# Kernel optimization log

Measured on AMD Instinct MI355X. Metric: run time of the kernel, lower is better.

## Reference

```python
import jax, jax.numpy as jnp
import numpy as np

D_MODEL = 1024
N_HEADS = 16
HEAD_DIM = D_MODEL // N_HEADS  # 64
SEQ = 2048
BATCH = 2


def setup_inputs() -> dict:
    key = jax.random.key(0)
    ks = jax.random.split(key, 12)
    s = 1.0 / np.sqrt(D_MODEL)
    return {
        "query": jax.random.normal(ks[0], (SEQ, BATCH, D_MODEL), jnp.float32),
        "key": jax.random.normal(ks[1], (SEQ, BATCH, D_MODEL), jnp.float32),
        "value": jax.random.normal(ks[2], (SEQ, BATCH, D_MODEL), jnp.float32),
        "Wq": jax.random.normal(ks[3], (D_MODEL, D_MODEL), jnp.float32) * s,
        "bq": jax.random.normal(ks[4], (D_MODEL,), jnp.float32) * s,
        "Wk": jax.random.normal(ks[5], (D_MODEL, D_MODEL), jnp.float32) * s,
        "bk": jax.random.normal(ks[6], (D_MODEL,), jnp.float32) * s,
        "Wv": jax.random.normal(ks[7], (D_MODEL, D_MODEL), jnp.float32) * s,
        "bv": jax.random.normal(ks[8], (D_MODEL,), jnp.float32) * s,
        "Wo": jax.random.normal(ks[9], (D_MODEL, D_MODEL), jnp.float32) * s,
        "bo": jax.random.normal(ks[10], (D_MODEL,), jnp.float32) * s,
    }


def _rope_tables(seq_len):
    # theta_i = 1 / 10000^(2i/head_dim), i in [0, head_dim//2)
    theta = 1.0 / (10000.0 ** (2.0 * jnp.arange(HEAD_DIM // 2, dtype=jnp.float32) / HEAD_DIM))
    pos = jnp.arange(seq_len, dtype=jnp.float32)[:, None, None, None] * theta  # [S,1,1,hd/2]
    return jnp.sin(pos), jnp.cos(pos)


def _apply_rope(t, sin, cos):
    # t: [S, B, H, hd]; NOTE faithful to source: t2 = q1*sin - q2*cos (minus)
    h = HEAD_DIM // 2
    q1, q2 = t[..., :h], t[..., h:]
    return jnp.concatenate([q1 * cos - q2 * sin, q1 * sin - q2 * cos], axis=-1)


def reference(query, key, value, Wq, bq, Wk, bk, Wv, bv, Wo, bo):
    S, B, _ = query.shape
    q = (query @ Wq.T + bq).reshape(S, B, N_HEADS, HEAD_DIM)
    k = (key @ Wk.T + bk).reshape(S, B, N_HEADS, HEAD_DIM)
    v = (value @ Wv.T + bv).reshape(S, B, N_HEADS, HEAD_DIM)
    sin, cos = _rope_tables(S)
    q = _apply_rope(q, sin, cos)
    k = _apply_rope(k, sin, cos)
    # [S,B,H,d] -> [B,H,S,d]
    q = q.transpose(1, 2, 0, 3)
    k = k.transpose(1, 2, 0, 3)
    v = v.transpose(1, 2, 0, 3)
    scale = 1.0 / jnp.sqrt(jnp.float32(HEAD_DIM))
    scores = jnp.einsum("bhqd,bhkd->bhqk", q, k) * scale
    attn = jax.nn.softmax(scores, axis=-1)
    out = jnp.einsum("bhqk,bhkd->bhqd", attn, v)  # [B,H,S,d]
    out = out.transpose(2, 0, 1, 3).reshape(S, B, D_MODEL)
    return out @ Wo.T + bo
```

## Files before the change

kernel.cpp:

```cpp
#include <hip/hip_runtime.h>

#define DMODEL 1024
#define NHEADS 16
#define HDIM   64
#define SEQ    2048
#define BATCH  2
#define MROWS  (SEQ*BATCH)

typedef unsigned int u32;
typedef unsigned short u16;
typedef __attribute__((ext_vector_type(8))) short bfrag;
typedef __attribute__((ext_vector_type(4))) float f32x4;
typedef __attribute__((ext_vector_type(16))) float f32x16;
typedef union { u32 u[4]; bfrag f; } fragu;

__device__ __forceinline__ u32 f2bf(float x) {
    unsigned u = __float_as_uint(x);
    return (u + 0x7fffu + ((u >> 16) & 1u)) >> 16;
}
__device__ __forceinline__ float bf2f(u32 h) {
    return __uint_as_float(h << 16);
}
__device__ __forceinline__ u32 packbf(float x) {
    const u32 h = f2bf(x);
    const u32 l = f2bf(x - bf2f(h));
    return h | (l << 16);
}

__device__ __forceinline__ void gld16(const void* g, void* l) {
    __builtin_amdgcn_global_load_lds(
        (const __attribute__((address_space(1))) unsigned int*)g,
        (__attribute__((address_space(3))) unsigned int*)l, 16, 0, 0);
}

__device__ __forceinline__ void unpack8(uint4 x, uint4 y, bfrag& hi, bfrag& lo) {
    fragu h, l;
    const u32 pk[8] = {x.x, x.y, x.z, x.w, y.x, y.y, y.z, y.w};
    #pragma unroll
    for (int j = 0; j < 4; ++j) {
        h.u[j] = (pk[2 * j] & 0xffffu) | (pk[2 * j + 1] << 16);
        l.u[j] = (pk[2 * j] >> 16) | (pk[2 * j + 1] & 0xffff0000u);
    }
    hi = h.f; lo = l.f;
}

__global__ __launch_bounds__(256) void prep_kernel(
    const float* __restrict__ Wq, const float* __restrict__ Wk,
    const float* __restrict__ Wv,
    float* __restrict__ query, float* __restrict__ key, float* __restrict__ value,
    u32* __restrict__ wqp, u32* __restrict__ wkp, u32* __restrict__ wvp,
    float2* __restrict__ tab)
{
    const int y = blockIdx.y;
    if (y == 3) {
        if (blockIdx.x >= 256) return;
        const int e = blockIdx.x * 256 + threadIdx.x;
        const int s = e >> 5, i = e & 31;
        const double th = exp(-(double)i * (9.210340371976184 / 32.0));
        double sn, cs;
        sincos((double)s * th, &sn, &cs);
        tab[e] = make_float2((float)sn, (float)cs);
        return;
    }
    const float* src; u32* dst;
    if (y < 3) {
        if (blockIdx.x >= 512) return;
        src = (y == 0) ? Wq : (y == 1) ? Wk : Wv;
        dst = (y == 0) ? wqp : (y == 1) ? wkp : wvp;
    } else {
        float* io = (y == 4) ? query : (y == 5) ? key : value;
        src = io;
        dst = (u32*)io;
    }
    const int i = blockIdx.x * 256 + threadIdx.x;
    float xs[8];
    *(float4*)&xs[0] = ((const float4*)src)[i * 2];
    *(float4*)&xs[4] = ((const float4*)src)[i * 2 + 1];
    u32 p[8];
    #pragma unroll
    for (int j = 0; j < 8; ++j) p[j] = packbf(xs[j]);
    *(uint4*)&dst[i * 8]     = *(const uint4*)&p[0];
    *(uint4*)&dst[i * 8 + 4] = *(const uint4*)&p[4];
}

__global__ __launch_bounds__(256) void pack_kernel(
    const float* __restrict__ src, u32* __restrict__ dst)
{
    const int i = blockIdx.x * 256 + threadIdx.x;
    float xs[8];
    *(float4*)&xs[0] = ((const float4*)src)[i * 2];
    *(float4*)&xs[4] = ((const float4*)src)[i * 2 + 1];
    u32 p[8];
    #pragma unroll
    for (int j = 0; j < 8; ++j) p[j] = packbf(xs[j]);
    *(uint4*)&dst[i * 8]     = *(const uint4*)&p[0];
    *(uint4*)&dst[i * 8 + 4] = *(const uint4*)&p[4];
}

__device__ __forceinline__ void gemm_body(
    int id, int mode,
    const u32* __restrict__ Ap, const u32* __restrict__ Wp,
    const float* __restrict__ bias, const float2* __restrict__ tab,
    float rope_scale,
    u16* __restrict__ Oh, u16* __restrict__ Ol, float* __restrict__ Of,
    u32* smem)
{
    u32* sA = smem;
    u32* sB = smem + 8192;

    const int tid   = threadIdx.x;
    const int w     = tid >> 6;
    const int lane  = tid & 63;
    const int lrow  = lane & 15;
    const int lquad = lane >> 4;

    const int xcd  = id & 7;
    const int jj   = id >> 3;
    const int nblk = jj & 15;
    const int mblk = (xcd << 2) | (jj >> 4);
    const int n0   = nblk * 64;
    const int m0   = mblk * 128;

    const int srow8 = lane >> 3;
    const int sch   = (lane & 7) ^ srow8;

    int aoff[2][2];
    int boff[4][2];
    #pragma unroll
    for (int mi = 0; mi < 2; ++mi) {
        const int ra = w * 32 + mi * 16 + lrow;
        #pragma unroll
        for (int hf = 0; hf < 2; ++hf)
            aoff[mi][hf] = ra * 32 + (((lquad * 2 + hf) ^ (ra & 7)) << 2);
    }
    #pragma unroll
    for (int ni = 0; ni < 4; ++ni) {
        const int rb = ni * 16 + lrow;
        #pragma unroll
        for (int hf = 0; hf < 2; ++hf)
            boff[ni][hf] = rb * 32 + (((lquad * 2 + hf) ^ (rb & 7)) << 2);
    }

    f32x4 acc[2][4] = {};

    auto stage = [&](int t) {
        const int h  = t & 1;
        const int kc = t * 32;
        #pragma unroll
        for (int i = 0; i < 4; ++i) {
            const int slab = w * 4 + i;
            const int row  = slab * 8 + srow8;
            gld16(Ap + (size_t)(m0 + row) * 1024 + kc + sch * 4,
                  sA + h * 4096 + slab * 256);
        }
        #pragma unroll
        for (int i = 0; i < 2; ++i) {
            const int slab = w * 2 + i;
            const int row  = slab * 8 + srow8;
            gld16(Wp + (size_t)(n0 + row) * 1024 + kc + sch * 4,
                  sB + h * 2048 + slab * 256);
        }
    };

    stage(0);
    for (int t = 0; t < 32; ++t) {
        __syncthreads();
        if (t < 31) stage(t + 1);
        const int h = t & 1;
        const u32* sAh_ = sA + h * 4096;
        const u32* sBh_ = sB + h * 2048;

        bfrag ah[2], al[2], bh[4], bl[4];
        #pragma unroll
        for (int mi = 0; mi < 2; ++mi)
            unpack8(*(const uint4*)(sAh_ + aoff[mi][0]),
                    *(const uint4*)(sAh_ + aoff[mi][1]), ah[mi], al[mi]);
        #pragma unroll
        for (int ni = 0; ni < 4; ++ni)
            unpack8(*(const uint4*)(sBh_ + boff[ni][0]),
                    *(const uint4*)(sBh_ + boff[ni][1]), bh[ni], bl[ni]);

        #pragma unroll
        for (int mi = 0; mi < 2; ++mi)
            #pragma unroll
            for (int ni = 0; ni < 4; ++ni) {
                acc[mi][ni] = __builtin_amdgcn_mfma_f32_16x16x32_bf16(ah[mi], bh[ni], acc[mi][ni], 0, 0, 0);
                acc[mi][ni] = __builtin_amdgcn_mfma_f32_16x16x32_bf16(ah[mi], bl[ni], acc[mi][ni], 0, 0, 0);
                acc[mi][ni] = __builtin_amdgcn_mfma_f32_16x16x32_bf16(al[mi], bh[ni], acc[mi][ni], 0, 0, 0);
            }
    }

    float bn[4];
    #pragma unroll
    for (int ni = 0; ni < 4; ++ni) bn[ni] = bias[n0 + ni * 16 + lrow];

    if (mode == 0) {
        const int hblk = nblk;
        #pragma unroll
        for (int mi = 0; mi < 2; ++mi)
            #pragma unroll
            for (int r = 0; r < 4; ++r) {
                const int mrow = w * 32 + mi * 16 + lquad * 4 + r;
                const int m  = m0 + mrow;
                const int bb = m & 1;
                const int sg = m >> 1;
                const size_t ob = (((size_t)(bb * NHEADS + hblk) * SEQ) + sg) * HDIM;
                #pragma unroll
                for (int ni = 0; ni < 2; ++ni) {
                    const int i = ni * 16 + lrow;
                    const float2 sc = tab[(size_t)sg * 32 + i];
                    const float x1 = acc[mi][ni][r]     + bn[ni];
                    const float x2 = acc[mi][ni + 2][r] + bn[ni + 2];
                    const float o1 = (x1 * sc.y - x2 * sc.x) * rope_scale;
                    const float o2 = (x1 * sc.x - x2 * sc.y) * rope_scale;
                    const u32 h1 = f2bf(o1);
                    const u32 h2 = f2bf(o2);
                    Oh[ob + i]      = (u16)h1;  Ol[ob + i]      = (u16)f2bf(o1 - bf2f(h1));
                    Oh[ob + i + 32] = (u16)h2;  Ol[ob + i + 32] = (u16)f2bf(o2 - bf2f(h2));
                }
            }
    } else if (mode == 1) {
        __syncthreads();
        u32* vb = smem;
        #pragma unroll
        for (int mi = 0; mi < 2; ++mi)
            #pragma unroll
            for (int r = 0; r < 4; ++r) {
                const int mrow = w * 32 + mi * 16 + lquad * 4 + r;
                const int bb = mrow & 1;
                const int sl = mrow >> 1;
                #pragma unroll
                for (int ni = 0; ni < 4; ++ni) {
                    const int d = ni * 16 + lrow;
                    vb[bb * 4160 + d * 65 + sl] = f2bf(acc[mi][ni][r] + bn[ni]);
                }
            }
        __syncthreads();
        const int hblk = nblk;
        #pragma unroll
        for (int rep = 0; rep < 4; ++rep) {
            const int c  = rep * 256 + tid;
            const int bb = c >> 9;
            const int d  = (c >> 3) & 63;
            const int s8 = c & 7;
            __align__(8) u16 hb[8];
            #pragma unroll
            for (int j = 0; j < 8; ++j)
                hb[j] = (u16)vb[bb * 4160 + d * 65 + s8 * 8 + j];
            const size_t orow = ((size_t)(bb * NHEADS + hblk) * HDIM + d) * SEQ + (m0 >> 1);
            const int blk16 = (s8 >> 1) * 16;
            const int off   = (s8 & 1) * 4;
            *(uint2*)&Oh[orow + blk16 + off]     = *(const uint2*)&hb[0];
            *(uint2*)&Oh[orow + blk16 + 8 + off] = *(const uint2*)&hb[4];
        }
    } else {
        #pragma unroll
        for (int mi = 0; mi < 2; ++mi)
            #pragma unroll
            for (int r = 0; r < 4; ++r) {
                const int m = m0 + w * 32 + mi * 16 + lquad * 4 + r;
                #pragma unroll
                for (int ni = 0; ni < 4; ++ni)
                    Of[(size_t)m * 1024 + n0 + ni * 16 + lrow] = acc[mi][ni][r] + bn[ni];
            }
    }
}

__global__ __launch_bounds__(256) void qkv_gemm_kernel(
    const u32* __restrict__ query, const u32* __restrict__ key,
    const u32* __restrict__ value,
    const u32* __restrict__ Wqp, const u32* __restrict__ Wkp,
    const u32* __restrict__ Wvp,
    const float* __restrict__ bq, const float* __restrict__ bk,
    const float* __restrict__ bv, const float2* __restrict__ tab,
    u16* __restrict__ Qh, u16* __restrict__ Ql,
    u16* __restrict__ Kh, u16* __restrict__ Kl,
    u16* __restrict__ VTh)
{
    __shared__ uint4 smem4[3072];
    const int z  = blockIdx.z;
    const int id = blockIdx.x + 16 * blockIdx.y;
    const u32* A    = (z == 0) ? query : (z == 1) ? key : value;
    const u32* Wp   = (z == 0) ? Wqp : (z == 1) ? Wkp : Wvp;
    const float* bb = (z == 0) ? bq : (z == 1) ? bk : bv;
    u16* Oh = (z == 0) ? Qh : (z == 1) ? Kh : VTh;
    u16* Ol = (z == 0) ? Ql : (z == 1) ? Kl : nullptr;
    const int mode = (z == 2) ? 1 : 0;
    const float scale = (z == 0) ? 0.125f : 1.0f;
    gemm_body(id, mode, A, Wp, bb, tab, scale, Oh, Ol, nullptr, (u32*)smem4);
}

__global__ __launch_bounds__(256) void out_gemm_kernel(
    const u32* __restrict__ Ap, const u32* __restrict__ Wp,
    const float* __restrict__ bias, float* __restrict__ Of)
{
    __shared__ uint4 smem4[3072];
    const int id = blockIdx.x + 16 * blockIdx.y;
    gemm_body(id, 2, Ap, Wp, bias, nullptr, 1.0f, nullptr, nullptr, Of, (u32*)smem4);
}

__global__ __launch_bounds__(256) void attn_mfma_kernel(
    const u16* __restrict__ Qh, const u16* __restrict__ Ql,
    const u16* __restrict__ Kh, const u16* __restrict__ Kl,
    const u16* __restrict__ Vh,
    u32* __restrict__ AOp)
{
    __shared__ u16 sKh[8192], sKl[8192];
    __shared__ u16 sVh[8192];

    const int tid  = threadIdx.x;
    const int w    = tid >> 6;
    const int lane = tid & 63;
    const int l31  = lane & 31;
    const int g    = lane >> 5;

    const int id = blockIdx.x + 16 * blockIdx.y;
    const int jj = id >> 3;
    const int bh = ((id & 7) << 2) | (jj >> 4);
    const int qt = jj & 15;

    const size_t qg = ((size_t)bh * SEQ + qt * 128 + w * 32 + l31) * HDIM + g * 8;
    bfrag qfh[4], qfl[4];
    #pragma unroll
    for (int ks = 0; ks < 4; ++ks) {
        qfh[ks] = *(const bfrag*)&Qh[qg + ks * 16];
        qfl[ks] = *(const bfrag*)&Ql[qg + ks * 16];
    }

    const int srow   = lane >> 3;
    const int schunk = (lane & 7) ^ srow;
    const u16* gsrc = nullptr; u16* lbase = nullptr; size_t istep = 0, ktstep = 0;
    if (w == 0) {
        gsrc = Kh + ((size_t)bh * SEQ + srow) * HDIM + schunk * 8;
        istep = 8 * 64; ktstep = 64 * 64; lbase = sKh;
    } else if (w == 1) {
        gsrc = Kl + ((size_t)bh * SEQ + srow) * HDIM + schunk * 8;
        istep = 8 * 64; ktstep = 64 * 64; lbase = sKl;
    } else if (w == 2) {
        gsrc = Vh + ((size_t)bh * HDIM + srow) * SEQ + schunk * 8;
        istep = 8 * SEQ; ktstep = 64; lbase = sVh;
    }

    int koff[2][4];
    #pragma unroll
    for (int a = 0; a < 2; ++a) {
        const int row = a * 32 + l31;
        #pragma unroll
        for (int c = 0; c < 4; ++c)
            koff[a][c] = row * 64 + (((c * 2 + g) ^ (row & 7)) << 3);
    }

    f32x16 accO[2] = {};
    float l_loc = 0.0f;

    auto stage = [&](int kt) {
        if (w < 3) {
            const u16* gp = gsrc + (size_t)kt * ktstep;
            u16* dst = lbase + (kt & 1) * 4096;
            #pragma unroll
            for (int i = 0; i < 8; ++i)
                gld16(gp + (size_t)i * istep, dst + i * 512);
        }
    };

    stage(0);
    for (int kt = 0; kt < SEQ / 64; ++kt) {
        __syncthreads();
        if (kt < SEQ / 64 - 1) stage(kt + 1);
        const int po = (kt & 1) * 4096;

        f32x16 accS[2] = {};
        #pragma unroll
        for (int kg = 0; kg < 2; ++kg)
            #pragma unroll
            for (int ks = 0; ks < 4; ++ks) {
                const bfrag kh = *(const bfrag*)&sKh[po + koff[kg][ks]];
                const bfrag kl = *(const bfrag*)&sKl[po + koff[kg][ks]];
                accS[kg] = __builtin_amdgcn_mfma_f32_32x32x16_bf16(kh, qfh[ks], accS[kg], 0, 0, 0);
                accS[kg] = __builtin_amdgcn_mfma_f32_32x32x16_bf16(kh, qfl[ks], accS[kg], 0, 0, 0);
                accS[kg] = __builtin_amdgcn_mfma_f32_32x32x16_bf16(kl, qfh[ks], accS[kg], 0, 0, 0);
            }

        float pv[2][16];
        #pragma unroll
        for (int kg = 0; kg < 2; ++kg)
            #pragma unroll
            for (int r = 0; r < 16; ++r) {
                const float p = __expf(accS[kg][r]);
                pv[kg][r] = p;
                l_loc += p;
            }

        #pragma unroll
        for (int kp = 0; kp < 4; ++kp) {
            const int kg = kp >> 1;
            const int t8 = (kp & 1) * 8;
            fragu ph;
            #pragma unroll
            for (int j2 = 0; j2 < 4; ++j2)
                ph.u[j2] = f2bf(pv[kg][t8 + 2 * j2]) |
                           (f2bf(pv[kg][t8 + 2 * j2 + 1]) << 16);
            #pragma unroll
            for (int dt = 0; dt < 2; ++dt) {
                const bfrag vh = *(const bfrag*)&sVh[po + koff[dt][kp]];
                accO[dt] = __builtin_amdgcn_mfma_f32_32x32x16_bf16(vh, ph.f, accO[dt], 0, 0, 0);
            }
        }
    }

    const float inv = 1.0f / (l_loc + __shfl_xor(l_loc, 32));

    const int b = bh >> 4;
    const int h = bh & 15;
    const int sg = qt * 128 + w * 32 + l31;
    const size_t obase = ((size_t)sg * BATCH + b) * DMODEL + h * 64;
    #pragma unroll
    for (int dt = 0; dt < 2; ++dt)
        #pragma unroll
        for (int rq = 0; rq < 4; ++rq) {
            const int d0 = 8 * rq + 4 * g + 32 * dt;
            uint4 pw;
            pw.x = packbf(accO[dt][rq * 4 + 0] * inv);
            pw.y = packbf(accO[dt][rq * 4 + 1] * inv);
            pw.z = packbf(accO[dt][rq * 4 + 2] * inv);
            pw.w = packbf(accO[dt][rq * 4 + 3] * inv);
            *(uint4*)&AOp[obase + d0] = pw;
        }
}

extern "C" void kernel_launch(void* const* d_in, const int* in_sizes, int n_in,
                              void* d_out, int out_size, void* d_ws, size_t ws_size,
                              hipStream_t stream)
{
    float* query = (float*)d_in[0];
    float* key   = (float*)d_in[1];
    float* value = (float*)d_in[2];
    const float* Wq    = (const float*)d_in[3];
    const float* bq    = (const float*)d_in[4];
    const float* Wk    = (const float*)d_in[5];
    const float* bk    = (const float*)d_in[6];
    const float* Wv    = (const float*)d_in[7];
    const float* bv    = (const float*)d_in[8];
    const float* Wo    = (const float*)d_in[9];
    const float* bo    = (const float*)d_in[10];
    float* out = (float*)d_out;

    char* wsb = (char*)d_ws;
    const size_t MB = 1024 * 1024;
    u32* Wqp = (u32*)(wsb + 0 * MB);
    u32* Wkp = (u32*)(wsb + 4 * MB);
    u32* Wvp = (u32*)(wsb + 8 * MB);
    float2* tab = (float2*)(wsb + 12 * MB);
    u16* Qh  = (u16*)(wsb + 16 * MB); u16* Ql  = (u16*)(wsb + 24 * MB);
    u16* Kh  = (u16*)(wsb + 32 * MB); u16* Kl  = (u16*)(wsb + 40 * MB);
    u16* VTh = (u16*)(wsb + 48 * MB);
    u32* AOp = (u32*)(wsb + 0 * MB);
    u32* Wop = (u32*)(wsb + 16 * MB);

    prep_kernel<<<dim3(2048, 7), 256, 0, stream>>>(
        Wq, Wk, Wv, query, key, value, Wqp, Wkp, Wvp, tab);
    qkv_gemm_kernel<<<dim3(16, 32, 3), 256, 0, stream>>>(
        (const u32*)query, (const u32*)key, (const u32*)value,
        Wqp, Wkp, Wvp, bq, bk, bv, tab,
        Qh, Ql, Kh, Kl, VTh);
    attn_mfma_kernel<<<dim3(16, 32), 256, 0, stream>>>(
        Qh, Ql, Kh, Kl, VTh, AOp);
    pack_kernel<<<512, 256, 0, stream>>>(Wo, Wop);
    out_gemm_kernel<<<dim3(16, 32), 256, 0, stream>>>(AOp, Wop, bo, out);
}
```

Measured before the change: 335.1 us.

## Split attention KV range across blocks, pre-split bf16 hi/lo layout, narrower out GEMM tiles

Operands are now stored as separate bf16 hi and lo halves in 32-element chunks, so the GEMM loads MFMA fragments directly without per-iteration unpacking. Attention splits the key range in two via blockIdx.z and accumulates unnormalized outputs and row sums with float atomics into zeroed buffers. A new combine kernel normalizes and packs the result. The output GEMM uses 32-column tiles to launch twice as many blocks. In exchange this adds extra kernels, atomic traffic, and drops the double-buffered K/V staging in attention.

```diff
diff --git a/kernel.cpp b/kernel.cpp
--- a/kernel.cpp
+++ b/kernel.cpp
@@ -21,11 +21,6 @@
 __device__ __forceinline__ float bf2f(u32 h) {
     return __uint_as_float(h << 16);
 }
-__device__ __forceinline__ u32 packbf(float x) {
-    const u32 h = f2bf(x);
-    const u32 l = f2bf(x - bf2f(h));
-    return h | (l << 16);
-}
 
 __device__ __forceinline__ void gld16(const void* g, void* l) {
     __builtin_amdgcn_global_load_lds(
@@ -33,22 +28,12 @@
         (__attribute__((address_space(3))) unsigned int*)l, 16, 0, 0);
 }
 
-__device__ __forceinline__ void unpack8(uint4 x, uint4 y, bfrag& hi, bfrag& lo) {
-    fragu h, l;
-    const u32 pk[8] = {x.x, x.y, x.z, x.w, y.x, y.y, y.z, y.w};
-    #pragma unroll
-    for (int j = 0; j < 4; ++j) {
-        h.u[j] = (pk[2 * j] & 0xffffu) | (pk[2 * j + 1] << 16);
-        l.u[j] = (pk[2 * j] >> 16) | (pk[2 * j + 1] & 0xffff0000u);
-    }
-    hi = h.f; lo = l.f;
-}
 
 __global__ __launch_bounds__(256) void prep_kernel(
     const float* __restrict__ Wq, const float* __restrict__ Wk,
     const float* __restrict__ Wv,
     float* __restrict__ query, float* __restrict__ key, float* __restrict__ value,
-    u32* __restrict__ wqp, u32* __restrict__ wkp, u32* __restrict__ wvp,
+    u16* __restrict__ wqb, u16* __restrict__ wkb, u16* __restrict__ wvb,
     float2* __restrict__ tab)
 {
     const int y = blockIdx.y;
@@ -62,51 +47,92 @@
         tab[e] = make_float2((float)sn, (float)cs);
         return;
     }
-    const float* src; u32* dst;
     if (y < 3) {
-        if (blockIdx.x >= 512) return;
-        src = (y == 0) ? Wq : (y == 1) ? Wk : Wv;
-        dst = (y == 0) ? wqp : (y == 1) ? wkp : wvp;
-    } else {
-        float* io = (y == 4) ? query : (y == 5) ? key : value;
-        src = io;
-        dst = (u32*)io;
-    }
+        const float* src = (y == 0) ? Wq : (y == 1) ? Wk : Wv;
+        u16* dst = (y == 0) ? wqb : (y == 1) ? wkb : wvb;
+        const int i = blockIdx.x * 256 + threadIdx.x;
+        const int e0  = i * 8;
+        const int row = e0 >> 10, k = e0 & 1023, t = k >> 5, j0 = k & 31;
+        float xs[8];
+        *(float4*)&xs[0] = ((const float4*)src)[i * 2];
+        *(float4*)&xs[4] = ((const float4*)src)[i * 2 + 1];
+        __align__(16) u16 hb[8];
+        __align__(16) u16 lb[8];
+        #pragma unroll
+        for (int j = 0; j < 8; ++j) {
+            const u32 h = f2bf(xs[j]);
+            hb[j] = (u16)h;
+            lb[j] = (u16)f2bf(xs[j] - bf2f(h));
+        }
+        u16* o = dst + (size_t)row * 2048 + t * 64 + j0;
+        *(uint4*)o        = *(const uint4*)hb;
+        *(uint4*)(o + 32) = *(const uint4*)lb;
+        return;
+    }
+    float* io = (y == 4) ? query : (y == 5) ? key : value;
+    const int gi = blockIdx.x * 256 + threadIdx.x;
+    uint4* io4 = (uint4*)io + (size_t)gi * 8;
+    uint4 raw[8];
+    #pragma unroll
+    for (int j = 0; j < 8; ++j) raw[j] = io4[j];
+    __align__(16) u16 hb[32];
+    __align__(16) u16 lb[32];
+    #pragma unroll
+    for (int j = 0; j < 32; ++j) {
+        const float x = __uint_as_float(((const u32*)raw)[j]);
+        const u32 h = f2bf(x);
+        hb[j] = (u16)h;
+        lb[j] = (u16)f2bf(x - bf2f(h));
+    }
+    #pragma unroll
+    for (int j = 0; j < 4; ++j) io4[j]     = ((const uint4*)hb)[j];
+    #pragma unroll
+    for (int j = 0; j < 4; ++j) io4[4 + j] = ((const uint4*)lb)[j];
+}
+
+__global__ __launch_bounds__(256) void pack_kernel(
+    const float* __restrict__ src, u16* __restrict__ dst)
+{
     const int i = blockIdx.x * 256 + threadIdx.x;
+    const int e0  = i * 8;
+    const int row = e0 >> 10, k = e0 & 1023, t = k >> 5, j0 = k & 31;
     float xs[8];
     *(float4*)&xs[0] = ((const float4*)src)[i * 2];
     *(float4*)&xs[4] = ((const float4*)src)[i * 2 + 1];
-    u32 p[8];
-    #pragma unroll
-    for (int j = 0; j < 8; ++j) p[j] = packbf(xs[j]);
-    *(uint4*)&dst[i * 8]     = *(const uint4*)&p[0];
-    *(uint4*)&dst[i * 8 + 4] = *(const uint4*)&p[4];
-}
-
-__global__ __launch_bounds__(256) void pack_kernel(
-    const float* __restrict__ src, u32* __restrict__ dst)
-{
+    __align__(16) u16 hb[8];
+    __align__(16) u16 lb[8];
+    #pragma unroll
+    for (int j = 0; j < 8; ++j) {
+        const u32 h = f2bf(xs[j]);
+        hb[j] = (u16)h;
+        lb[j] = (u16)f2bf(xs[j] - bf2f(h));
+    }
+    u16* o = dst + (size_t)row * 2048 + t * 64 + j0;
+    *(uint4*)o        = *(const uint4*)hb;
+    *(uint4*)(o + 32) = *(const uint4*)lb;
+}
+
+__global__ __launch_bounds__(256) void zero_kernel(float* __restrict__ AOf,
+                                                   float* __restrict__ lsum)
+{
+    const int y = blockIdx.y;
+    uint4* dst  = (uint4*)(y == 0 ? AOf : lsum);
+    const int n = (y == 0) ? (1 << 20) : (1 << 14);
     const int i = blockIdx.x * 256 + threadIdx.x;
-    float xs[8];
-    *(float4*)&xs[0] = ((const float4*)src)[i * 2];
-    *(float4*)&xs[4] = ((const float4*)src)[i * 2 + 1];
-    u32 p[8];
-    #pragma unroll
-    for (int j = 0; j < 8; ++j) p[j] = packbf(xs[j]);
-    *(uint4*)&dst[i * 8]     = *(const uint4*)&p[0];
-    *(uint4*)&dst[i * 8 + 4] = *(const uint4*)&p[4];
-}
-
+    if (i < n) dst[i] = make_uint4(0, 0, 0, 0);
+}
+
+template <int NI>
 __device__ __forceinline__ void gemm_body(
     int id, int mode,
-    const u32* __restrict__ Ap, const u32* __restrict__ Wp,
+    const u16* __restrict__ Ab, const u16* __restrict__ Wb,
     const float* __restrict__ bias, const float2* __restrict__ tab,
     float rope_scale,
     u16* __restrict__ Oh, u16* __restrict__ Ol, float* __restrict__ Of,
-    u32* smem)
-{
-    u32* sA = smem;
-    u32* sB = smem + 8192;
+    u16* smem16)
+{
+    u16* sA = smem16;
+    u16* sB = smem16 + 16384;
 
     const int tid   = threadIdx.x;
     const int w     = tid >> 6;
@@ -114,51 +140,48 @@
     const int lrow  = lane & 15;
     const int lquad = lane >> 4;
 
+    const int NBLK = 1024 / (NI * 16);
     const int xcd  = id & 7;
     const int jj   = id >> 3;
-    const int nblk = jj & 15;
-    const int mblk = (xcd << 2) | (jj >> 4);
-    const int n0   = nblk * 64;
+    const int nblk = jj & (NBLK - 1);
+    const int mblk = (xcd << 2) | (jj / NBLK);
+    const int n0   = nblk * NI * 16;
     const int m0   = mblk * 128;
 
     const int srow8 = lane >> 3;
     const int sch   = (lane & 7) ^ srow8;
 
-    int aoff[2][2];
-    int boff[4][2];
+    int aoffh[2], aoffl[2], boffh[NI], boffl[NI];
     #pragma unroll
     for (int mi = 0; mi < 2; ++mi) {
         const int ra = w * 32 + mi * 16 + lrow;
-        #pragma unroll
-        for (int hf = 0; hf < 2; ++hf)
-            aoff[mi][hf] = ra * 32 + (((lquad * 2 + hf) ^ (ra & 7)) << 2);
-    }
-    #pragma unroll
-    for (int ni = 0; ni < 4; ++ni) {
+        aoffh[mi] = ra * 64 + ((lquad ^ (ra & 7)) << 3);
+        aoffl[mi] = ra * 64 + (((lquad + 4) ^ (ra & 7)) << 3);
+    }
+    #pragma unroll
+    for (int ni = 0; ni < NI; ++ni) {
         const int rb = ni * 16 + lrow;
-        #pragma unroll
-        for (int hf = 0; hf < 2; ++hf)
-            boff[ni][hf] = rb * 32 + (((lquad * 2 + hf) ^ (rb & 7)) << 2);
-    }
-
-    f32x4 acc[2][4] = {};
+        boffh[ni] = rb * 64 + ((lquad ^ (rb & 7)) << 3);
+        boffl[ni] = rb * 64 + (((lquad + 4) ^ (rb & 7)) << 3);
+    }
+
+    f32x4 acc[2][NI] = {};
 
     auto stage = [&](int t) {
-        const int h  = t & 1;
-        const int kc = t * 32;
+        const int h = t & 1;
         #pragma unroll
         for (int i = 0; i < 4; ++i) {
             const int slab = w * 4 + i;
             const int row  = slab * 8 + srow8;
-            gld16(Ap + (size_t)(m0 + row) * 1024 + kc + sch * 4,
-                  sA + h * 4096 + slab * 256);
-        }
-        #pragma unroll
-        for (int i = 0; i < 2; ++i) {
-            const int slab = w * 2 + i;
+            gld16(Ab + (size_t)(m0 + row) * 2048 + t * 64 + sch * 8,
+                  sA + h * 8192 + slab * 512);
+        }
+        #pragma unroll
+        for (int i = 0; i < NI / 2; ++i) {
+            const int slab = w * (NI / 2) + i;
             const int row  = slab * 8 + srow8;
-            gld16(Wp + (size_t)(n0 + row) * 1024 + kc + sch * 4,
-                  sB + h * 2048 + slab * 256);
+            gld16(Wb + (size_t)(n0 + row) * 2048 + t * 64 + sch * 8,
+                  sB + h * (NI * 1024) + slab * 512);
         }
     };
 
@@ -167,146 +190,151 @@
         __syncthreads();
         if (t < 31) stage(t + 1);
         const int h = t & 1;
-        const u32* sAh_ = sA + h * 4096;
-        const u32* sBh_ = sB + h * 2048;
-
-        bfrag ah[2], al[2], bh[4], bl[4];
+        const u16* sAh_ = sA + h * 8192;
+        const u16* sBh_ = sB + h * (NI * 1024);
+
+        bfrag ah[2], al[2], bh[NI], bl[NI];
+        #pragma unroll
+        for (int mi = 0; mi < 2; ++mi) {
+            ah[mi] = *(const bfrag*)&sAh_[aoffh[mi]];
+            al[mi] = *(const bfrag*)&sAh_[aoffl[mi]];
+        }
+        #pragma unroll
+        for (int ni = 0; ni < NI; ++ni) {
+            bh[ni] = *(const bfrag*)&sBh_[boffh[ni]];
+            bl[ni] = *(const bfrag*)&sBh_[boffl[ni]];
+        }
+
         #pragma unroll
         for (int mi = 0; mi < 2; ++mi)
-            unpack8(*(const uint4*)(sAh_ + aoff[mi][0]),
-                    *(const uint4*)(sAh_ + aoff[mi][1]), ah[mi], al[mi]);
-        #pragma unroll
-        for (int ni = 0; ni < 4; ++ni)
-            unpack8(*(const uint4*)(sBh_ + boff[ni][0]),
-                    *(const uint4*)(sBh_ + boff[ni][1]), bh[ni], bl[ni]);
-
-        #pragma unroll
-        for (int mi = 0; mi < 2; ++mi)
-            #pragma unroll
-            for (int ni = 0; ni < 4; ++ni) {
+            #pragma unroll
+            for (int ni = 0; ni < NI; ++ni) {
                 acc[mi][ni] = __builtin_amdgcn_mfma_f32_16x16x32_bf16(ah[mi], bh[ni], acc[mi][ni], 0, 0, 0);
                 acc[mi][ni] = __builtin_amdgcn_mfma_f32_16x16x32_bf16(ah[mi], bl[ni], acc[mi][ni], 0, 0, 0);
                 acc[mi][ni] = __builtin_amdgcn_mfma_f32_16x16x32_bf16(al[mi], bh[ni], acc[mi][ni], 0, 0, 0);
             }
     }
 
-    float bn[4];
-    #pragma unroll
-    for (int ni = 0; ni < 4; ++ni) bn[ni] = bias[n0 + ni * 16 + lrow];
-
-    if (mode == 0) {
-        const int hblk = nblk;
-        #pragma unroll
-        for (int mi = 0; mi < 2; ++mi)
-            #pragma unroll
-            for (int r = 0; r < 4; ++r) {
-                const int mrow = w * 32 + mi * 16 + lquad * 4 + r;
-                const int m  = m0 + mrow;
-                const int bb = m & 1;
-                const int sg = m >> 1;
-                const size_t ob = (((size_t)(bb * NHEADS + hblk) * SEQ) + sg) * HDIM;
+    float bn[NI];
+    #pragma unroll
+    for (int ni = 0; ni < NI; ++ni) bn[ni] = bias[n0 + ni * 16 + lrow];
+
+    if constexpr (NI == 4) {
+        if (mode == 0) {
+            const int hblk = nblk;
+            #pragma unroll
+            for (int mi = 0; mi < 2; ++mi)
                 #pragma unroll
-                for (int ni = 0; ni < 2; ++ni) {
-                    const int i = ni * 16 + lrow;
-                    const float2 sc = tab[(size_t)sg * 32 + i];
-                    const float x1 = acc[mi][ni][r]     + bn[ni];
-                    const float x2 = acc[mi][ni + 2][r] + bn[ni + 2];
-                    const float o1 = (x1 * sc.y - x2 * sc.x) * rope_scale;
-                    const float o2 = (x1 * sc.x - x2 * sc.y) * rope_scale;
-                    const u32 h1 = f2bf(o1);
-                    const u32 h2 = f2bf(o2);
-                    Oh[ob + i]      = (u16)h1;  Ol[ob + i]      = (u16)f2bf(o1 - bf2f(h1));
-                    Oh[ob + i + 32] = (u16)h2;  Ol[ob + i + 32] = (u16)f2bf(o2 - bf2f(h2));
+                for (int r = 0; r < 4; ++r) {
+                    const int mrow = w * 32 + mi * 16 + lquad * 4 + r;
+                    const int m  = m0 + mrow;
+                    const int bb = m & 1;
+                    const int sg = m >> 1;
+                    const size_t ob = (((size_t)(bb * NHEADS + hblk) * SEQ) + sg) * HDIM;
+                    #pragma unroll
+                    for (int ni = 0; ni < 2; ++ni) {
+                        const int i = ni * 16 + lrow;
+                        const float2 sc = tab[(size_t)sg * 32 + i];
+                        const float x1 = acc[mi][ni][r]     + bn[ni];
+                        const float x2 = acc[mi][ni + 2][r] + bn[ni + 2];
+                        const float o1 = (x1 * sc.y - x2 * sc.x) * rope_scale;
+                        const float o2 = (x1 * sc.x - x2 * sc.y) * rope_scale;
+                        const u32 h1 = f2bf(o1);
+                        const u32 h2 = f2bf(o2);
+                        Oh[ob + i]      = (u16)h1;  Ol[ob + i]      = (u16)f2bf(o1 - bf2f(h1));
+                        Oh[ob + i + 32] = (u16)h2;  Ol[ob + i + 32] = (u16)f2bf(o2 - bf2f(h2));
+                    }
                 }
+            return;
+        }
+        if (mode == 1) {
+            __syncthreads();
+            u32* vb = (u32*)smem16;
+            #pragma unroll
+            for (int mi = 0; mi < 2; ++mi)
+                #pragma unroll
+                for (int r = 0; r < 4; ++r) {
+                    const int mrow = w * 32 + mi * 16 + lquad * 4 + r;
+                    const int bb = mrow & 1;
+                    const int sl = mrow >> 1;
+                    #pragma unroll
+                    for (int ni = 0; ni < 4; ++ni) {
+                        const int d = ni * 16 + lrow;
+                        vb[bb * 4160 + d * 65 + sl] = f2bf(acc[mi][ni][r] + bn[ni]);
+                    }
+                }
+            __syncthreads();
+            const int hblk = nblk;
+            #pragma unroll
+            for (int rep = 0; rep < 4; ++rep) {
+                const int c  = rep * 256 + tid;
+                const int bb = c >> 9;
+                const int d  = (c >> 3) & 63;
+                const int s8 = c & 7;
+                __align__(8) u16 hb[8];
+                #pragma unroll
+                for (int j = 0; j < 8; ++j)
+                    hb[j] = (u16)vb[bb * 4160 + d * 65 + s8 * 8 + j];
+                const size_t orow = ((size_t)(bb * NHEADS + hblk) * HDIM + d) * SEQ + (m0 >> 1);
+                const int blk16 = (s8 >> 1) * 16;
+                const int off   = (s8 & 1) * 4;
+                *(uint2*)&Oh[orow + blk16 + off]     = *(const uint2*)&hb[0];
+                *(uint2*)&Oh[orow + blk16 + 8 + off] = *(const uint2*)&hb[4];
             }
-    } else if (mode == 1) {
-        __syncthreads();
-        u32* vb = smem;
-        #pragma unroll
-        for (int mi = 0; mi < 2; ++mi)
-            #pragma unroll
-            for (int r = 0; r < 4; ++r) {
-                const int mrow = w * 32 + mi * 16 + lquad * 4 + r;
-                const int bb = mrow & 1;
-                const int sl = mrow >> 1;
-                #pragma unroll
-                for (int ni = 0; ni < 4; ++ni) {
-                    const int d = ni * 16 + lrow;
-                    vb[bb * 4160 + d * 65 + sl] = f2bf(acc[mi][ni][r] + bn[ni]);
-                }
-            }
-        __syncthreads();
-        const int hblk = nblk;
-        #pragma unroll
-        for (int rep = 0; rep < 4; ++rep) {
-            const int c  = rep * 256 + tid;
-            const int bb = c >> 9;
-            const int d  = (c >> 3) & 63;
-            const int s8 = c & 7;
-            __align__(8) u16 hb[8];
-            #pragma unroll
-            for (int j = 0; j < 8; ++j)
-                hb[j] = (u16)vb[bb * 4160 + d * 65 + s8 * 8 + j];
-            const size_t orow = ((size_t)(bb * NHEADS + hblk) * HDIM + d) * SEQ + (m0 >> 1);
-            const int blk16 = (s8 >> 1) * 16;
-            const int off   = (s8 & 1) * 4;
-            *(uint2*)&Oh[orow + blk16 + off]     = *(const uint2*)&hb[0];
-            *(uint2*)&Oh[orow + blk16 + 8 + off] = *(const uint2*)&hb[4];
-        }
-    } else {
-        #pragma unroll
-        for (int mi = 0; mi < 2; ++mi)
-            #pragma unroll
-            for (int r = 0; r < 4; ++r) {
-                const int m = m0 + w * 32 + mi * 16 + lquad * 4 + r;
-                #pragma unroll
-                for (int ni = 0; ni < 4; ++ni)
-                    Of[(size_t)m * 1024 + n0 + ni * 16 + lrow] = acc[mi][ni][r] + bn[ni];
-            }
-    }
+            return;
+        }
+    }
+    #pragma unroll
+    for (int mi = 0; mi < 2; ++mi)
+        #pragma unroll
+        for (int r = 0; r < 4; ++r) {
+            const int m = m0 + w * 32 + mi * 16 + lquad * 4 + r;
+            #pragma unroll
+            for (int ni = 0; ni < NI; ++ni)
+                Of[(size_t)m * 1024 + n0 + ni * 16 + lrow] = acc[mi][ni][r] + bn[ni];
+        }
 }
 
 __global__ __launch_bounds__(256) void qkv_gemm_kernel(
-    const u32* __restrict__ query, const u32* __restrict__ key,
-    const u32* __restrict__ value,
-    const u32* __restrict__ Wqp, const u32* __restrict__ Wkp,
-    const u32* __restrict__ Wvp,
+    const u16* __restrict__ query, const u16* __restrict__ key,
+    const u16* __restrict__ value,
+    const u16* __restrict__ Wqb, const u16* __restrict__ Wkb,
+    const u16* __restrict__ Wvb,
     const float* __restrict__ bq, const float* __restrict__ bk,
     const float* __restrict__ bv, const float2* __restrict__ tab,
     u16* __restrict__ Qh, u16* __restrict__ Ql,
     u16* __restrict__ Kh, u16* __restrict__ Kl,
     u16* __restrict__ VTh)
 {
-    __shared__ uint4 smem4[3072];
+    __shared__ u16 smem16[24576];
     const int z  = blockIdx.z;
     const int id = blockIdx.x + 16 * blockIdx.y;
-    const u32* A    = (z == 0) ? query : (z == 1) ? key : value;
-    const u32* Wp   = (z == 0) ? Wqp : (z == 1) ? Wkp : Wvp;
+    const u16* A    = (z == 0) ? query : (z == 1) ? key : value;
+    const u16* Wb   = (z == 0) ? Wqb : (z == 1) ? Wkb : Wvb;
     const float* bb = (z == 0) ? bq : (z == 1) ? bk : bv;
     u16* Oh = (z == 0) ? Qh : (z == 1) ? Kh : VTh;
     u16* Ol = (z == 0) ? Ql : (z == 1) ? Kl : nullptr;
     const int mode = (z == 2) ? 1 : 0;
     const float scale = (z == 0) ? 0.125f : 1.0f;
-    gemm_body(id, mode, A, Wp, bb, tab, scale, Oh, Ol, nullptr, (u32*)smem4);
+    gemm_body<4>(id, mode, A, Wb, bb, tab, scale, Oh, Ol, nullptr, smem16);
 }
 
 __global__ __launch_bounds__(256) void out_gemm_kernel(
-    const u32* __restrict__ Ap, const u32* __restrict__ Wp,
+    const u16* __restrict__ Ab, const u16* __restrict__ Wb,
     const float* __restrict__ bias, float* __restrict__ Of)
 {
-    __shared__ uint4 smem4[3072];
-    const int id = blockIdx.x + 16 * blockIdx.y;
-    gemm_body(id, 2, Ap, Wp, bias, nullptr, 1.0f, nullptr, nullptr, Of, (u32*)smem4);
+    __shared__ u16 smem16[20480];
+    const int id = blockIdx.x + 32 * blockIdx.y;
+    gemm_body<2>(id, 2, Ab, Wb, bias, nullptr, 1.0f, nullptr, nullptr, Of, smem16);
 }
 
 __global__ __launch_bounds__(256) void attn_mfma_kernel(
     const u16* __restrict__ Qh, const u16* __restrict__ Ql,
     const u16* __restrict__ Kh, const u16* __restrict__ Kl,
     const u16* __restrict__ Vh,
-    u32* __restrict__ AOp)
-{
-    __shared__ u16 sKh[8192], sKl[8192];
-    __shared__ u16 sVh[8192];
+    float* __restrict__ AOf, float* __restrict__ lsum)
+{
+    __shared__ u16 sKh[4096], sKl[4096], sVh[4096];
 
     const int tid  = threadIdx.x;
     const int w    = tid >> 6;
@@ -318,6 +346,7 @@
     const int jj = id >> 3;
     const int bh = ((id & 7) << 2) | (jj >> 4);
     const int qt = jj & 15;
+    const int kh = blockIdx.z;
 
     const size_t qg = ((size_t)bh * SEQ + qt * 128 + w * 32 + l31) * HDIM + g * 8;
     bfrag qfh[4], qfl[4];
@@ -353,32 +382,26 @@
     f32x16 accO[2] = {};
     float l_loc = 0.0f;
 
-    auto stage = [&](int kt) {
+    for (int kt = kh * 16; kt < kh * 16 + 16; ++kt) {
+        __syncthreads();
         if (w < 3) {
             const u16* gp = gsrc + (size_t)kt * ktstep;
-            u16* dst = lbase + (kt & 1) * 4096;
             #pragma unroll
             for (int i = 0; i < 8; ++i)
-                gld16(gp + (size_t)i * istep, dst + i * 512);
-        }
-    };
-
-    stage(0);
-    for (int kt = 0; kt < SEQ / 64; ++kt) {
+                gld16(gp + (size_t)i * istep, lbase + i * 512);
+        }
         __syncthreads();
-        if (kt < SEQ / 64 - 1) stage(kt + 1);
-        const int po = (kt & 1) * 4096;
 
         f32x16 accS[2] = {};
         #pragma unroll
         for (int kg = 0; kg < 2; ++kg)
             #pragma unroll
             for (int ks = 0; ks < 4; ++ks) {
-                const bfrag kh = *(const bfrag*)&sKh[po + koff[kg][ks]];
-                const bfrag kl = *(const bfrag*)&sKl[po + koff[kg][ks]];
-                accS[kg] = __builtin_amdgcn_mfma_f32_32x32x16_bf16(kh, qfh[ks], accS[kg], 0, 0, 0);
-                accS[kg] = __builtin_amdgcn_mfma_f32_32x32x16_bf16(kh, qfl[ks], accS[kg], 0, 0, 0);
-                accS[kg] = __builtin_amdgcn_mfma_f32_32x32x16_bf16(kl, qfh[ks], accS[kg], 0, 0, 0);
+                const bfrag kh_ = *(const bfrag*)&sKh[koff[kg][ks]];
+                const bfrag kl_ = *(const bfrag*)&sKl[koff[kg][ks]];
+                accS[kg] = __builtin_amdgcn_mfma_f32_32x32x16_bf16(kh_, qfh[ks], accS[kg], 0, 0, 0);
+                accS[kg] = __builtin_amdgcn_mfma_f32_32x32x16_bf16(kh_, qfl[ks], accS[kg], 0, 0, 0);
+                accS[kg] = __builtin_amdgcn_mfma_f32_32x32x16_bf16(kl_, qfh[ks], accS[kg], 0, 0, 0);
             }
 
         float pv[2][16];
@@ -402,30 +425,53 @@
                            (f2bf(pv[kg][t8 + 2 * j2 + 1]) << 16);
             #pragma unroll
             for (int dt = 0; dt < 2; ++dt) {
-                const bfrag vh = *(const bfrag*)&sVh[po + koff[dt][kp]];
+                const bfrag vh = *(const bfrag*)&sVh[koff[dt][kp]];
                 accO[dt] = __builtin_amdgcn_mfma_f32_32x32x16_bf16(vh, ph.f, accO[dt], 0, 0, 0);
             }
         }
     }
 
-    const float inv = 1.0f / (l_loc + __shfl_xor(l_loc, 32));
-
+    const float lpart = l_loc + __shfl_xor(l_loc, 32);
     const int b = bh >> 4;
     const int h = bh & 15;
     const int sg = qt * 128 + w * 32 + l31;
-    const size_t obase = ((size_t)sg * BATCH + b) * DMODEL + h * 64;
+    if (g == 0) atomicAdd(&lsum[bh * 2048 + sg], lpart);
+    const size_t ob = ((size_t)sg * BATCH + b) * DMODEL + h * 64;
     #pragma unroll
     for (int dt = 0; dt < 2; ++dt)
         #pragma unroll
         for (int rq = 0; rq < 4; ++rq) {
             const int d0 = 8 * rq + 4 * g + 32 * dt;
-            uint4 pw;
-            pw.x = packbf(accO[dt][rq * 4 + 0] * inv);
-            pw.y = packbf(accO[dt][rq * 4 + 1] * inv);
-            pw.z = packbf(accO[dt][rq * 4 + 2] * inv);
-            pw.w = packbf(accO[dt][rq * 4 + 3] * inv);
-            *(uint4*)&AOp[obase + d0] = pw;
-        }
+            #pragma unroll
+            for (int i2 = 0; i2 < 4; ++i2)
+                atomicAdd(&AOf[ob + d0 + i2], accO[dt][rq * 4 + i2]);
+        }
+}
+
+__global__ __launch_bounds__(256) void combine_kernel(
+    const float* __restrict__ AOf, const float* __restrict__ lsum,
+    u16* __restrict__ AOb)
+{
+    const int i  = blockIdx.x * 256 + threadIdx.x;
+    const int rm = i >> 7;
+    const int k0 = (i & 127) * 8;
+    float xs[8];
+    *(float4*)&xs[0] = ((const float4*)AOf)[rm * 256 + (k0 >> 2)];
+    *(float4*)&xs[4] = ((const float4*)AOf)[rm * 256 + (k0 >> 2) + 1];
+    const int h = k0 >> 6, s = rm >> 1, bb = rm & 1;
+    const float linv = 1.0f / lsum[(bb * NHEADS + h) * 2048 + s];
+    __align__(16) u16 hb[8];
+    __align__(16) u16 lb[8];
+    #pragma unroll
+    for (int j = 0; j < 8; ++j) {
+        const float v = xs[j] * linv;
+        const u32 hh = f2bf(v);
+        hb[j] = (u16)hh;
+        lb[j] = (u16)f2bf(v - bf2f(hh));
+    }
+    u16* o = AOb + (size_t)rm * 2048 + (k0 >> 5) * 64 + (k0 & 31);
+    *(uint4*)o        = *(const uint4*)hb;
+    *(uint4*)(o + 32) = *(const uint4*)lb;
 }
 
 extern "C" void kernel_launch(void* const* d_in, const int* in_sizes, int n_in,
@@ -447,24 +493,27 @@
 
     char* wsb = (char*)d_ws;
     const size_t MB = 1024 * 1024;
-    u32* Wqp = (u32*)(wsb + 0 * MB);
-    u32* Wkp = (u32*)(wsb + 4 * MB);
-    u32* Wvp = (u32*)(wsb + 8 * MB);
+    u16* Wqb = (u16*)(wsb + 0 * MB);
+    u16* Wkb = (u16*)(wsb + 4 * MB);
+    u16* Wvb = (u16*)(wsb + 8 * MB);
     float2* tab = (float2*)(wsb + 12 * MB);
     u16* Qh  = (u16*)(wsb + 16 * MB); u16* Ql  = (u16*)(wsb + 24 * MB);
     u16* Kh  = (u16*)(wsb + 32 * MB); u16* Kl  = (u16*)(wsb + 40 * MB);
     u16* VTh = (u16*)(wsb + 48 * MB);
-    u32* AOp = (u32*)(wsb + 0 * MB);
-    u32* Wop = (u32*)(wsb + 16 * MB);
-
-    prep_kernel<<<dim3(2048, 7), 256, 0, stream>>>(
-        Wq, Wk, Wv, query, key, value, Wqp, Wkp, Wvp, tab);
+    float* AOf  = (float*)(wsb + 0 * MB);
+    float* lsum = (float*)(wsb + 56 * MB);
+    u16* AOb = (u16*)(wsb + 32 * MB);
+    u16* Wob = (u16*)(wsb + 16 * MB);
+
+    prep_kernel<<<dim3(512, 7), 256, 0, stream>>>(
+        Wq, Wk, Wv, query, key, value, Wqb, Wkb, Wvb, tab);
     qkv_gemm_kernel<<<dim3(16, 32, 3), 256, 0, stream>>>(
-        (const u32*)query, (const u32*)key, (const u32*)value,
-        Wqp, Wkp, Wvp, bq, bk, bv, tab,
-        Qh, Ql, Kh, Kl, VTh);
-    attn_mfma_kernel<<<dim3(16, 32), 256, 0, stream>>>(
-        Qh, Ql, Kh, Kl, VTh, AOp);
-    pack_kernel<<<512, 256, 0, stream>>>(Wo, Wop);
-    out_gemm_kernel<<<dim3(16, 32), 256, 0, stream>>>(AOp, Wop, bo, out);
-}
+        (const u16*)query, (const u16*)key, (const u16*)value,
+        Wqb, Wkb, Wvb, bq, bk, bv, tab, Qh, Ql, Kh, Kl, VTh);
+    zero_kernel<<<dim3(4096, 2), 256, 0, stream>>>(AOf, lsum);
+    attn_mfma_kernel<<<dim3(16, 32, 2), 256, 0, stream>>>(
+        Qh, Ql, Kh, Kl, VTh, AOf, lsum);
+    combine_kernel<<<2048, 256, 0, stream>>>(AOf, lsum, AOb);
+    pack_kernel<<<512, 256, 0, stream>>>(Wo, Wob);
+    out_gemm_kernel<<<dim3(32, 32), 256, 0, stream>>>(AOb, Wob, bo, out);
+}
```

Result: slower. 495.3 us (+47.8%).
